# Kernel tuning notes

Hardware: AMD Instinct MI355X
Metric: run time of the kernel (lower is better)

Reference implementation:

```python
import jax, jax.numpy as jnp
import numpy as np

N = 50000
E = 800000
NODE_CONT = 64
EDGE_CAT = 16
HID = 96
LAT = 64
NUM_LAYERS = 2
BN_EPS = 1e-5


def setup_inputs() -> dict:
    key = jax.random.key(0)
    ks = jax.random.split(key, 24)
    s = 0.05
    inp = {
        "x_cont": jax.random.normal(ks[0], (N, NODE_CONT), jnp.float32),
        "x_cat": jax.random.randint(ks[1], (N,), 0, 1),
        "edge_index": jax.random.randint(ks[2], (2, E), 0, N),
        "edge_attr_cat": jax.random.randint(ks[3], (E,), 0, EDGE_CAT),
        "edge_attr_cont": jax.random.normal(ks[4], (E, 1), jnp.float32),
        # parameters
        "w_node": jax.random.normal(ks[5], (HID, NODE_CONT), jnp.float32) * s,
        "b_node": jnp.zeros((HID,), jnp.float32),
        "edge_embed": jax.random.normal(ks[6], (EDGE_CAT, HID), jnp.float32) * s,
        "gcn_w": jax.random.normal(ks[7], (NUM_LAYERS, HID, HID), jnp.float32) * s,
        "gcn_b": jnp.zeros((NUM_LAYERS, HID), jnp.float32),
        "bn_gamma": jnp.ones((NUM_LAYERS, HID), jnp.float32),
        "bn_beta": jnp.zeros((NUM_LAYERS, HID), jnp.float32),
        "mlp_w1": jax.random.normal(ks[8], (NUM_LAYERS, HID, 2 * HID), jnp.float32) * s,
        "mlp_b1": jnp.zeros((NUM_LAYERS, HID), jnp.float32),
        "mlp_w2": jax.random.normal(ks[9], (NUM_LAYERS, HID, HID), jnp.float32) * s,
        "mlp_b2": jnp.zeros((NUM_LAYERS, HID), jnp.float32),
        "mu_w": jax.random.normal(ks[10], (LAT, HID), jnp.float32) * s,
        "mu_b": jnp.zeros((LAT,), jnp.float32),
        "lv_w": jax.random.normal(ks[11], (LAT, HID), jnp.float32) * s,
        "lv_b": jnp.zeros((LAT,), jnp.float32),
    }
    return inp


def _forward(x_cont, edge_index, edge_attr_cat,
             w_node, b_node, edge_embed,
             gcn_w, gcn_b, bn_gamma, bn_beta,
             mlp_w1, mlp_b1, mlp_w2, mlp_b2,
             mu_w, mu_b, lv_w, lv_b):
    n = x_cont.shape[0]
    # node embed (only continuous path active)
    h = x_cont @ w_node.T + b_node                      # [N, H]
    # edge embed (only categorical path active) -- memory-bound gather
    edge_h = edge_embed[edge_attr_cat]                  # [E, H]
    src, dst = edge_index[0], edge_index[1]
    # GCNConv: add self-loops, symmetric normalization
    loop = jnp.arange(n)
    src_f = jnp.concatenate([src, loop])
    dst_f = jnp.concatenate([dst, loop])
    deg = jax.ops.segment_sum(jnp.ones_like(dst_f, jnp.float32), dst_f, num_segments=n)
    dinv = jax.lax.rsqrt(deg)                           # deg >= 1 (self loops)
    norm = (dinv[src_f] * dinv[dst_f])[:, None]         # [E+N, 1]
    # edge_pooled: O(E) segment-mean replacing the O(N*E) python loop;
    # edge_h is constant across layers so compute it once.
    cnt = jax.ops.segment_sum(jnp.ones((edge_h.shape[0],), edge_h.dtype), dst, num_segments=n)
    pooled = jax.ops.segment_sum(edge_h, dst, num_segments=n) / jnp.maximum(cnt, 1.0)[:, None]
    for l in range(gcn_w.shape[0]):
        msg = (h @ gcn_w[l].T)[src_f] * norm            # gather + scale
        h_gnn = jax.ops.segment_sum(msg, dst_f, num_segments=n) + gcn_b[l]
        hc = jnp.concatenate([h_gnn, pooled], axis=-1)  # [N, 2H]
        h = jax.nn.relu(hc @ mlp_w1[l].T + mlp_b1[l]) @ mlp_w2[l].T + mlp_b2[l]
        # BatchNorm1d (training-mode batch stats, biased variance)
        mean = jnp.mean(h, axis=0)
        var = jnp.mean((h - mean) ** 2, axis=0)
        h = (h - mean) * jax.lax.rsqrt(var + BN_EPS) * bn_gamma[l] + bn_beta[l]
        h = jax.nn.relu(h)
        # dropout: eval mode (identity)
    mu = h @ mu_w.T + mu_b
    logvar = h @ lv_w.T + lv_b
    return mu, logvar


def reference(x_cont, x_cat, edge_index, edge_attr_cat, edge_attr_cont,
              w_node, b_node, edge_embed, gcn_w, gcn_b, bn_gamma, bn_beta,
              mlp_w1, mlp_b1, mlp_w2, mlp_b2, mu_w, mu_b, lv_w, lv_b):
    # x_cat and edge_attr_cont are unused: in_node_cat_dim=0, in_edge_cont_dim=0
    return _forward(x_cont, edge_index, edge_attr_cat,
                    w_node, b_node, edge_embed,
                    gcn_w, gcn_b, bn_gamma, bn_beta,
                    mlp_w1, mlp_b1, mlp_w2, mlp_b2,
                    mu_w, mu_b, lv_w, lv_b)
```

## Files before the change

kernel.cpp:

```cpp
#include <hip/hip_runtime.h>

#define N_NODES 50000
#define N_EDGES 800000
#define HID 96
#define NODE_CONT 64
#define LATD 64
#define EDGE_CATN 16
#define BN_EPS 1e-5f
#define CPAD 16
#define BCAP 48

typedef __attribute__((ext_vector_type(8))) short bf16x8;
typedef __attribute__((ext_vector_type(4))) float f32x4;

__device__ __forceinline__ unsigned short f2bf(float f) {
    union { float f; unsigned u; } c; c.f = f;
    unsigned r = (c.u + 0x7fffu + ((c.u >> 16) & 1u)) >> 16;
    return (unsigned short)r;
}
__device__ __forceinline__ float bf2f(unsigned short u) {
    union { unsigned u; float f; } c; c.u = ((unsigned)u) << 16;
    return c.f;
}

__global__ void k_build(const int* __restrict__ ei, const int* __restrict__ ecat,
                        int* __restrict__ cnt, int* __restrict__ csr) {
    int e = blockIdx.x * blockDim.x + threadIdx.x;
    if (e >= N_EDGES) return;
    int dst = ei[N_EDGES + e];
    int r = atomicAdd(&cnt[dst * CPAD], 1);
    if (r < BCAP) csr[dst * BCAP + r] = (ei[e] << 4) | (ecat[e] & 15);
}

__global__ void k_dinv(const int* __restrict__ cnt, float* __restrict__ dinv) {
    int n = blockIdx.x * blockDim.x + threadIdx.x;
    if (n >= N_NODES) return;
    dinv[n] = rsqrtf((float)(cnt[n * CPAD] + 1));
}

template<int POOL>
__global__ __launch_bounds__(256) void k_aggregate(
    const int* __restrict__ csr, const int* __restrict__ cnt,
    const unsigned short* __restrict__ bt, const float* __restrict__ dinv,
    const float* __restrict__ gcn_b, unsigned short* __restrict__ bg,
    const float* __restrict__ eemb, unsigned short* __restrict__ bp)
{
    __shared__ float s_eemb[EDGE_CATN * HID];
    if constexpr (POOL) {
        for (int i = threadIdx.x; i < EDGE_CATN * HID; i += 256)
            s_eemb[i] = eemb[i];
        __syncthreads();
    }
    int node = blockIdx.x * 8 + (threadIdx.x >> 5);
    int lane = threadIdx.x & 31;
    if (node >= N_NODES) return;
    float dd = dinv[node];
    const unsigned short* tn = bt + (size_t)node * HID;
    float a0 = bf2f(tn[lane]);
    float a1 = bf2f(tn[lane + 32]);
    float a2 = bf2f(tn[lane + 64]);
    float p0 = 0.f, p1 = 0.f, p2 = 0.f;
    int deg = cnt[node * CPAD];
    if (deg > BCAP) deg = BCAP;
    int beg = node * BCAP, end = beg + deg;
    int p = beg;
    for (; p + 4 <= end; p += 4) {
        int e0 = csr[p], e1 = csr[p + 1], e2 = csr[p + 2], e3 = csr[p + 3];
        const unsigned short* r0 = bt + (size_t)(e0 >> 4) * HID;
        const unsigned short* r1 = bt + (size_t)(e1 >> 4) * HID;
        const unsigned short* r2 = bt + (size_t)(e2 >> 4) * HID;
        const unsigned short* r3 = bt + (size_t)(e3 >> 4) * HID;
        unsigned short v00 = r0[lane], v01 = r0[lane + 32], v02 = r0[lane + 64];
        unsigned short v10 = r1[lane], v11 = r1[lane + 32], v12 = r1[lane + 64];
        unsigned short v20 = r2[lane], v21 = r2[lane + 32], v22 = r2[lane + 64];
        unsigned short v30 = r3[lane], v31 = r3[lane + 32], v32 = r3[lane + 64];
        a0 += (bf2f(v00) + bf2f(v10)) + (bf2f(v20) + bf2f(v30));
        a1 += (bf2f(v01) + bf2f(v11)) + (bf2f(v21) + bf2f(v31));
        a2 += (bf2f(v02) + bf2f(v12)) + (bf2f(v22) + bf2f(v32));
        if constexpr (POOL) {
            const float* q0 = s_eemb + (e0 & 15) * HID;
            const float* q1 = s_eemb + (e1 & 15) * HID;
            const float* q2 = s_eemb + (e2 & 15) * HID;
            const float* q3 = s_eemb + (e3 & 15) * HID;
            p0 += (q0[lane] + q1[lane]) + (q2[lane] + q3[lane]);
            p1 += (q0[lane + 32] + q1[lane + 32]) + (q2[lane + 32] + q3[lane + 32]);
            p2 += (q0[lane + 64] + q1[lane + 64]) + (q2[lane + 64] + q3[lane + 64]);
        }
    }
    for (; p < end; ++p) {
        int e0 = csr[p];
        const unsigned short* r = bt + (size_t)(e0 >> 4) * HID;
        a0 += bf2f(r[lane]);
        a1 += bf2f(r[lane + 32]);
        a2 += bf2f(r[lane + 64]);
        if constexpr (POOL) {
            const float* q = s_eemb + (e0 & 15) * HID;
            p0 += q[lane]; p1 += q[lane + 32]; p2 += q[lane + 64];
        }
    }
    unsigned short* o = bg + (size_t)node * HID;
    o[lane]      = f2bf(a0 * dd + gcn_b[lane]);
    o[lane + 32] = f2bf(a1 * dd + gcn_b[lane + 32]);
    o[lane + 64] = f2bf(a2 * dd + gcn_b[lane + 64]);
    if constexpr (POOL) {
        float inv = 1.f / (float)(deg < 1 ? 1 : deg);
        unsigned short* ob = bp + (size_t)node * HID;
        ob[lane]      = f2bf(p0 * inv);
        ob[lane + 32] = f2bf(p1 * inv);
        ob[lane + 64] = f2bf(p2 * inv);
    }
}

#define OFF_WNODE 0
#define OFF_GCN   6144
#define OFF_W1    24576
#define OFF_W2    61440
#define OFF_MU    79872
#define OFF_LV    86016
#define W_TOTAL   92160

__global__ void k_wconv(const float* __restrict__ w_node, const float* __restrict__ gcn_w,
                        const float* __restrict__ w1, const float* __restrict__ w2,
                        const float* __restrict__ mu_w, const float* __restrict__ lv_w,
                        unsigned short* __restrict__ out) {
    int i = blockIdx.x * blockDim.x + threadIdx.x;
    if (i >= W_TOTAL) return;
    float v;
    if (i < OFF_GCN)      v = w_node[i - OFF_WNODE];
    else if (i < OFF_W1)  v = gcn_w[i - OFF_GCN];
    else if (i < OFF_W2)  v = w1[i - OFF_W1];
    else if (i < OFF_MU)  v = w2[i - OFF_W2];
    else if (i < OFF_LV)  v = mu_w[i - OFF_MU];
    else                  v = lv_w[i - OFF_LV];
    out[i] = f2bf(v);
}

__global__ void k_wfuse(const float* __restrict__ gcn_w, const float* __restrict__ w_node,
                        const float* __restrict__ b_node,
                        unsigned short* __restrict__ wbf, float* __restrict__ fused_b) {
    int i = blockIdx.x * blockDim.x + threadIdx.x;
    if (i < HID * NODE_CONT) {
        int j = i / NODE_CONT, k = i - j * NODE_CONT;
        float s = 0.f;
#pragma unroll 8
        for (int q = 0; q < HID; ++q) s += gcn_w[j * HID + q] * w_node[q * NODE_CONT + k];
        wbf[OFF_WNODE + i] = f2bf(s);
    } else if (i < HID * NODE_CONT + HID) {
        int j = i - HID * NODE_CONT;
        float s = 0.f;
#pragma unroll 8
        for (int q = 0; q < HID; ++q) s += gcn_w[j * HID + q] * b_node[q];
        fused_b[j] = s;
    }
}

template<int NJT, int AF32>
__global__ __launch_bounds__(320) void k_gemm_bf(
    const void* __restrict__ A1v, int K1,
    const unsigned short* __restrict__ A2, int K2,
    const float* __restrict__ ss,
    const unsigned short* __restrict__ Wb,
    const float* __restrict__ bias, const float* __restrict__ bias2,
    const float* __restrict__ rowscale,
    unsigned short* __restrict__ Yb, float* __restrict__ Yf, float* __restrict__ Yf2,
    int act)
{
    const int K = K1 + K2;
    const int tile = blockIdx.x * 5 + (threadIdx.x >> 6);
    const int lane = threadIdx.x & 63;
    const int m = lane & 15;
    const int kg = lane >> 4;

    f32x4 acc[NJT];
#pragma unroll
    for (int jt = 0; jt < NJT; ++jt) acc[jt] = (f32x4){0.f, 0.f, 0.f, 0.f};

    const int arow = tile * 16 + m;

    for (int k0 = 0; k0 < K; k0 += 32) {
        int gk = k0 + kg * 8;
        bf16x8 a;
        if constexpr (AF32) {
            const float* apf = (const float*)A1v + (size_t)arow * K1 + gk;
            float4 x0 = *reinterpret_cast<const float4*>(apf);
            float4 x1 = *reinterpret_cast<const float4*>(apf + 4);
            a[0] = f2bf(x0.x); a[1] = f2bf(x0.y); a[2] = f2bf(x0.z); a[3] = f2bf(x0.w);
            a[4] = f2bf(x1.x); a[5] = f2bf(x1.y); a[6] = f2bf(x1.z); a[7] = f2bf(x1.w);
        } else {
            const unsigned short* A1 = (const unsigned short*)A1v;
            const unsigned short* ap = (gk < K1) ? A1 + (size_t)arow * K1 + gk
                                                 : A2 + (size_t)arow * K2 + (gk - K1);
            a = *reinterpret_cast<const bf16x8*>(ap);
            if (ss) {
#pragma unroll
                for (int i = 0; i < 8; ++i) {
                    float v = bf2f((unsigned short)a[i]);
                    v = fmaxf(v * ss[gk + i] + ss[96 + gk + i], 0.f);
                    a[i] = (short)f2bf(v);
                }
            }
        }
#pragma unroll
        for (int jt = 0; jt < NJT; ++jt) {
            const unsigned short* wp = Wb + (size_t)(jt * 16 + m) * K + gk;
            bf16x8 b = *reinterpret_cast<const bf16x8*>(wp);
            acc[jt] = __builtin_amdgcn_mfma_f32_16x16x32_bf16(a, b, acc[jt], 0, 0, 0);
        }
    }

    const int crow = tile * 16 + kg * 4;
    float rs[4] = {1.f, 1.f, 1.f, 1.f};
    if (rowscale) {
#pragma unroll
        for (int r = 0; r < 4; ++r) rs[r] = rowscale[crow + r];
    }
#pragma unroll
    for (int jt = 0; jt < NJT; ++jt) {
        int j = jt * 16 + m;
        float bv = 0.f;
        if (Yf2) bv = (jt < NJT / 2) ? bias[j] : bias2[j - (NJT / 2) * 16];
        else if (bias) bv = bias[j];
#pragma unroll
        for (int r = 0; r < 4; ++r) {
            float v = acc[jt][r] + bv;
            if (act) v = fmaxf(v, 0.f);
            v *= rs[r];
            int row = crow + r;
            if (Yf2) {
                if (jt < NJT / 2) Yf[(size_t)row * ((NJT / 2) * 16) + j] = v;
                else              Yf2[(size_t)row * ((NJT / 2) * 16) + (j - (NJT / 2) * 16)] = v;
            } else {
                Yb[(size_t)row * (NJT * 16) + j] = f2bf(v);
            }
        }
    }
}

__global__ __launch_bounds__(320) void k_mlp(
    const unsigned short* __restrict__ A1, const unsigned short* __restrict__ A2,
    const unsigned short* __restrict__ W1, const float* __restrict__ b1,
    const unsigned short* __restrict__ W2, const float* __restrict__ b2,
    unsigned short* __restrict__ bh, float* __restrict__ stats)
{
    __shared__ float s_stat[192];
    __shared__ unsigned short s_z1[5][16][104];
    for (int j = threadIdx.x; j < 192; j += 320) s_stat[j] = 0.f;
    const int wid = threadIdx.x >> 6;
    const int tile = blockIdx.x * 5 + wid;
    const int lane = threadIdx.x & 63;
    const int m = lane & 15;
    const int kg = lane >> 4;
    const int arow = tile * 16 + m;

    f32x4 acc[6];
#pragma unroll
    for (int jt = 0; jt < 6; ++jt) acc[jt] = (f32x4){0.f, 0.f, 0.f, 0.f};

    for (int k0 = 0; k0 < 192; k0 += 32) {
        int gk = k0 + kg * 8;
        const unsigned short* ap = (gk < 96) ? A1 + (size_t)arow * 96 + gk
                                             : A2 + (size_t)arow * 96 + (gk - 96);
        bf16x8 a = *reinterpret_cast<const bf16x8*>(ap);
#pragma unroll
        for (int jt = 0; jt < 6; ++jt) {
            bf16x8 b = *reinterpret_cast<const bf16x8*>(W1 + (size_t)(jt * 16 + m) * 192 + gk);
            acc[jt] = __builtin_amdgcn_mfma_f32_16x16x32_bf16(a, b, acc[jt], 0, 0, 0);
        }
    }
#pragma unroll
    for (int jt = 0; jt < 6; ++jt) {
        int j = jt * 16 + m;
        float bv = b1[j];
#pragma unroll
        for (int r = 0; r < 4; ++r)
            s_z1[wid][kg * 4 + r][j] = f2bf(fmaxf(acc[jt][r] + bv, 0.f));
    }
    __syncthreads();

    f32x4 acc2[6];
#pragma unroll
    for (int jt = 0; jt < 6; ++jt) acc2[jt] = (f32x4){0.f, 0.f, 0.f, 0.f};
    for (int k0 = 0; k0 < 96; k0 += 32) {
        int gk = k0 + kg * 8;
        bf16x8 a = *reinterpret_cast<const bf16x8*>(&s_z1[wid][m][gk]);
#pragma unroll
        for (int jt = 0; jt < 6; ++jt) {
            bf16x8 b = *reinterpret_cast<const bf16x8*>(W2 + (size_t)(jt * 16 + m) * 96 + gk);
            acc2[jt] = __builtin_amdgcn_mfma_f32_16x16x32_bf16(a, b, acc2[jt], 0, 0, 0);
        }
    }
    const int crow = tile * 16 + kg * 4;
#pragma unroll
    for (int jt = 0; jt < 6; ++jt) {
        int j = jt * 16 + m;
        float bv = b2[j];
        float lsum = 0.f, lsq = 0.f;
#pragma unroll
        for (int r = 0; r < 4; ++r) {
            float v = acc2[jt][r] + bv;
            lsum += v; lsq += v * v;
            bh[(size_t)(crow + r) * HID + j] = f2bf(v);
        }
        atomicAdd(&s_stat[j], lsum);
        atomicAdd(&s_stat[96 + j], lsq);
    }
    __syncthreads();
    for (int j = threadIdx.x; j < 192; j += 320) atomicAdd(&stats[j], s_stat[j]);
}

__global__ void k_bn_finalize(const float* __restrict__ stats,
                              const float* __restrict__ g, const float* __restrict__ b,
                              float* __restrict__ ss) {
    int j = threadIdx.x;
    if (j >= 96) return;
    float mean = stats[j] / (float)N_NODES;
    float var = stats[96 + j] / (float)N_NODES - mean * mean;
    float sc = g[j] * rsqrtf(var + BN_EPS);
    ss[j] = sc;
    ss[96 + j] = b[j] - mean * sc;
}

extern "C" void kernel_launch(void* const* d_in, const int* in_sizes, int n_in,
                              void* d_out, int out_size, void* d_ws, size_t ws_size,
                              hipStream_t stream) {
    const float* x_cont = (const float*)d_in[0];
    const int* edge_index = (const int*)d_in[2];
    const int* ecat = (const int*)d_in[3];
    const float* w_node = (const float*)d_in[5];
    const float* b_node = (const float*)d_in[6];
    const float* eemb = (const float*)d_in[7];
    const float* gcn_w = (const float*)d_in[8];
    const float* gcn_b = (const float*)d_in[9];
    const float* bn_g = (const float*)d_in[10];
    const float* bn_b = (const float*)d_in[11];
    const float* w1 = (const float*)d_in[12];
    const float* b1 = (const float*)d_in[13];
    const float* w2 = (const float*)d_in[14];
    const float* b2 = (const float*)d_in[15];
    const float* mu_w = (const float*)d_in[16];
    const float* mu_b = (const float*)d_in[17];
    const float* lv_w = (const float*)d_in[18];
    const float* lv_b = (const float*)d_in[19];
    float* out = (float*)d_out;

    char* base = (char*)d_ws;
    float* dinv    = (float*)base;                      base += (size_t)N_NODES * 4;
    float* statsA  = (float*)base;                      base += 2 * 192 * 4;
    float* ssbuf   = (float*)base;                      base += 2 * 192 * 4;
    float* fused_b = (float*)base;                      base += 128 * 4;
    int*   cnt     = (int*)base;                        base += (size_t)N_NODES * CPAD * 4;
    int*   csr     = (int*)base;                        base += (size_t)N_NODES * BCAP * 4;
    unsigned short* wbf = (unsigned short*)base;        base += (size_t)W_TOTAL * 2;
    unsigned short* bh  = (unsigned short*)base;        base += (size_t)N_NODES * HID * 2;
    unsigned short* bt  = (unsigned short*)base;        base += (size_t)N_NODES * HID * 2;
    unsigned short* bg  = (unsigned short*)base;        base += (size_t)N_NODES * HID * 2;
    unsigned short* bp  = (unsigned short*)base;        base += (size_t)N_NODES * HID * 2;

    hipMemsetAsync(cnt, 0, (size_t)N_NODES * CPAD * sizeof(int), stream);
    hipMemsetAsync(statsA, 0, 2 * 192 * sizeof(float), stream);

    k_wconv<<<(W_TOTAL + 255) / 256, 256, 0, stream>>>(w_node, gcn_w, w1, w2, mu_w, lv_w, wbf);
    k_wfuse<<<(HID * NODE_CONT + HID + 255) / 256, 256, 0, stream>>>(gcn_w, w_node, b_node,
                                                                     wbf, fused_b);
    k_build<<<(N_EDGES + 255) / 256, 256, 0, stream>>>(edge_index, ecat, cnt, csr);
    k_dinv<<<(N_NODES + 255) / 256, 256, 0, stream>>>(cnt, dinv);

    const int GG = N_NODES / 16 / 5;

    for (int l = 0; l < 2; ++l) {
        if (l == 0)
            k_gemm_bf<6, 1><<<GG, 320, 0, stream>>>(x_cont, NODE_CONT, nullptr, 0, nullptr,
                                                    wbf + OFF_WNODE, fused_b, nullptr, dinv,
                                                    bt, nullptr, nullptr, 0);
        else
            k_gemm_bf<6, 0><<<GG, 320, 0, stream>>>(bh, HID, nullptr, 0, ssbuf,
                                                    wbf + OFF_GCN + l * HID * HID,
                                                    nullptr, nullptr, dinv,
                                                    bt, nullptr, nullptr, 0);
        if (l == 0)
            k_aggregate<1><<<N_NODES / 8, 256, 0, stream>>>(
                csr, cnt, bt, dinv, gcn_b + l * HID, bg, eemb, bp);
        else
            k_aggregate<0><<<N_NODES / 8, 256, 0, stream>>>(
                csr, cnt, bt, dinv, gcn_b + l * HID, bg, eemb, bp);
        k_mlp<<<GG, 320, 0, stream>>>(bg, bp,
                                      wbf + OFF_W1 + l * HID * 2 * HID, b1 + l * HID,
                                      wbf + OFF_W2 + l * HID * HID, b2 + l * HID,
                                      bh, statsA + l * 192);
        k_bn_finalize<<<1, 128, 0, stream>>>(statsA + l * 192, bn_g + l * HID, bn_b + l * HID,
                                             ssbuf + l * 192);
    }

    k_gemm_bf<8, 0><<<GG, 320, 0, stream>>>(bh, HID, nullptr, 0, ssbuf + 192,
                                            wbf + OFF_MU, mu_b, lv_b, nullptr,
                                            nullptr, out, out + (size_t)N_NODES * LATD, 0);
}
```

Measured before the change: 255.9 us.

## Partition CSR build by XCD node range and merge weight prep kernels

Result: faster. 246.4 us (-3.7%).

```diff
diff --git a/kernel.cpp b/kernel.cpp
--- a/kernel.cpp
+++ b/kernel.cpp
@@ -9,6 +9,10 @@
 #define BN_EPS 1e-5f
 #define CPAD 16
 #define BCAP 48
+#define NXCD 8
+#define NODES_PER_XCD (N_NODES / NXCD)
+#define BUILD_SUBS 128
+#define EDGES_PER_SUB (N_EDGES / BUILD_SUBS)
 
 typedef __attribute__((ext_vector_type(8))) short bf16x8;
 typedef __attribute__((ext_vector_type(4))) float f32x4;
@@ -23,13 +27,22 @@
     return c.f;
 }
 
-__global__ void k_build(const int* __restrict__ ei, const int* __restrict__ ecat,
-                        int* __restrict__ cnt, int* __restrict__ csr) {
-    int e = blockIdx.x * blockDim.x + threadIdx.x;
-    if (e >= N_EDGES) return;
-    int dst = ei[N_EDGES + e];
-    int r = atomicAdd(&cnt[dst * CPAD], 1);
-    if (r < BCAP) csr[dst * BCAP + r] = (ei[e] << 4) | (ecat[e] & 15);
+__global__ __launch_bounds__(256) void k_build(
+    const int* __restrict__ ei, const int* __restrict__ ecat,
+    int* __restrict__ cnt, int* __restrict__ csr)
+{
+    int xcd = blockIdx.x & (NXCD - 1);
+    int sub = blockIdx.x >> 3;
+    int lo = xcd * NODES_PER_XCD;
+    int hi = lo + NODES_PER_XCD;
+    int e1 = sub * EDGES_PER_SUB + EDGES_PER_SUB;
+    for (int e = sub * EDGES_PER_SUB + threadIdx.x; e < e1; e += 256) {
+        int dst = ei[N_EDGES + e];
+        if (dst >= lo && dst < hi) {
+            int r = atomicAdd(&cnt[dst * CPAD], 1);
+            if (r < BCAP) csr[dst * BCAP + r] = (ei[e] << 4) | (ecat[e] & 15);
+        }
+    }
 }
 
 __global__ void k_dinv(const int* __restrict__ cnt, float* __restrict__ dinv) {
@@ -119,38 +132,32 @@
 #define OFF_LV    86016
 #define W_TOTAL   92160
 
-__global__ void k_wconv(const float* __restrict__ w_node, const float* __restrict__ gcn_w,
+__global__ void k_wprep(const float* __restrict__ w_node, const float* __restrict__ gcn_w,
                         const float* __restrict__ w1, const float* __restrict__ w2,
                         const float* __restrict__ mu_w, const float* __restrict__ lv_w,
-                        unsigned short* __restrict__ out) {
-    int i = blockIdx.x * blockDim.x + threadIdx.x;
-    if (i >= W_TOTAL) return;
-    float v;
-    if (i < OFF_GCN)      v = w_node[i - OFF_WNODE];
-    else if (i < OFF_W1)  v = gcn_w[i - OFF_GCN];
-    else if (i < OFF_W2)  v = w1[i - OFF_W1];
-    else if (i < OFF_MU)  v = w2[i - OFF_W2];
-    else if (i < OFF_LV)  v = mu_w[i - OFF_MU];
-    else                  v = lv_w[i - OFF_LV];
-    out[i] = f2bf(v);
-}
-
-__global__ void k_wfuse(const float* __restrict__ gcn_w, const float* __restrict__ w_node,
                         const float* __restrict__ b_node,
-                        unsigned short* __restrict__ wbf, float* __restrict__ fused_b) {
+                        unsigned short* __restrict__ out, float* __restrict__ fused_b) {
     int i = blockIdx.x * blockDim.x + threadIdx.x;
     if (i < HID * NODE_CONT) {
         int j = i / NODE_CONT, k = i - j * NODE_CONT;
         float s = 0.f;
 #pragma unroll 8
         for (int q = 0; q < HID; ++q) s += gcn_w[j * HID + q] * w_node[q * NODE_CONT + k];
-        wbf[OFF_WNODE + i] = f2bf(s);
-    } else if (i < HID * NODE_CONT + HID) {
-        int j = i - HID * NODE_CONT;
-        float s = 0.f;
+        out[OFF_WNODE + i] = f2bf(s);
+        if (k == 0) {
+            float sb = 0.f;
 #pragma unroll 8
-        for (int q = 0; q < HID; ++q) s += gcn_w[j * HID + q] * b_node[q];
-        fused_b[j] = s;
+            for (int q = 0; q < HID; ++q) sb += gcn_w[j * HID + q] * b_node[q];
+            fused_b[j] = sb;
+        }
+    } else if (i < W_TOTAL) {
+        float v;
+        if (i < OFF_W1)       v = gcn_w[i - OFF_GCN];
+        else if (i < OFF_W2)  v = w1[i - OFF_W1];
+        else if (i < OFF_MU)  v = w2[i - OFF_W2];
+        else if (i < OFF_LV)  v = mu_w[i - OFF_MU];
+        else                  v = lv_w[i - OFF_LV];
+        out[i] = f2bf(v);
     }
 }
 
@@ -359,10 +366,9 @@
     hipMemsetAsync(cnt, 0, (size_t)N_NODES * CPAD * sizeof(int), stream);
     hipMemsetAsync(statsA, 0, 2 * 192 * sizeof(float), stream);
 
-    k_wconv<<<(W_TOTAL + 255) / 256, 256, 0, stream>>>(w_node, gcn_w, w1, w2, mu_w, lv_w, wbf);
-    k_wfuse<<<(HID * NODE_CONT + HID + 255) / 256, 256, 0, stream>>>(gcn_w, w_node, b_node,
-                                                                     wbf, fused_b);
-    k_build<<<(N_EDGES + 255) / 256, 256, 0, stream>>>(edge_index, ecat, cnt, csr);
+    k_wprep<<<(W_TOTAL + 255) / 256, 256, 0, stream>>>(w_node, gcn_w, w1, w2, mu_w, lv_w,
+                                                       b_node, wbf, fused_b);
+    k_build<<<NXCD * BUILD_SUBS, 256, 0, stream>>>(edge_index, ecat, cnt, csr);
     k_dinv<<<(N_NODES + 255) / 256, 256, 0, stream>>>(cnt, dinv);
 
     const int GG = N_NODES / 16 / 5;
```
